# Kernel optimization log

Hardware: AMD Instinct MI355X
Metric: run time of the kernel (lower is better)

## Reference

```python
import jax, jax.numpy as jnp
import numpy as np

B, L, D, H, E = 32, 100, 128, 8, 64
C = D // H
NEG_SLOPE = 0.2
MASK_VAL = -1e9
LN_EPS = 1e-5


def _glorot(key, shape):
    fan_in, fan_out = shape[-1], shape[-2]
    std = np.sqrt(6.0 / (fan_in + fan_out))
    return jax.random.uniform(key, shape, jnp.float32, -std, std)


def setup_inputs() -> dict:
    key = jax.random.key(0)
    ks = jax.random.split(key, 12)
    x = jax.random.normal(ks[0], (B, L, D), jnp.float32)
    adj = jax.random.randint(ks[1], (B, L, L), 0, 2, jnp.int32)
    e = jax.random.normal(ks[2], (B, L, L, E), jnp.float32)
    Wx = _glorot(ks[3], (D, D))          # linear_x weight (out, in)
    We = _glorot(ks[4], (D, E))          # linear_e weight (out, in)
    att_src = _glorot(ks[5], (H, C))
    att_dst = _glorot(ks[6], (H, C))
    att_e = _glorot(ks[7], (H, C))
    ffn_w = _glorot(ks[8], (D, D))
    ffn_b = jnp.zeros((D,), jnp.float32)
    ln_g = jnp.ones((D,), jnp.float32)
    ln_b = jnp.zeros((D,), jnp.float32)
    return dict(x=x, adj=adj, e=e, Wx=Wx, We=We, att_src=att_src,
                att_dst=att_dst, att_e=att_e, ffn_w=ffn_w, ffn_b=ffn_b,
                ln_g=ln_g, ln_b=ln_b)


def reference(x, adj, e, Wx, We, att_src, att_dst, att_e, ffn_w, ffn_b, ln_g, ln_b):
    Bb, Ll, Dd = x.shape
    Hh, Cc = att_src.shape
    # node / edge projections
    xp = (x @ Wx.T).reshape(Bb, Ll, Hh, Cc)                      # (B,L,H,C)
    ep = jnp.einsum('bije,de->bijd', e, We).reshape(Bb, Ll, Ll, Hh, Cc)  # (B,L,L,H,C)
    # per-head attention logits
    xj = jnp.einsum('blhc,hc->blh', xp, att_src)                 # source score
    xi = jnp.einsum('blhc,hc->blh', xp, att_dst)                 # dest score
    es = jnp.einsum('bijhc,hc->bijh', ep, att_e)                 # edge score
    s = xi[:, :, None, :] + xj[:, None, :, :] + es               # (B,L,L,H)
    s = jax.nn.leaky_relu(s, NEG_SLOPE)
    s = jnp.where((adj != 0)[..., None], s, MASK_VAL)
    alpha = jax.nn.softmax(s, axis=2)                            # softmax over j
    # aggregation: out[b,i,h,c] = sum_j alpha[b,i,j,h] * xp[b,j,h,c]
    out = jnp.einsum('bijh,bjhc->bihc', alpha, xp).reshape(Bb, Ll, Dd)
    # FFN: linear -> layernorm -> relu (dropout p=0)
    h = out @ ffn_w.T + ffn_b
    mu = h.mean(-1, keepdims=True)
    var = jnp.mean((h - mu) ** 2, axis=-1, keepdims=True)
    h = (h - mu) * jax.lax.rsqrt(var + LN_EPS) * ln_g + ln_b
    return jax.nn.relu(h)
```

## Files before the change

kernel.cpp:

```cpp
#include <hip/hip_runtime.h>
#include <hip/hip_bf16.h>

#define NB 32
#define NL 100
#define ND 128
#define NH 8
#define NE 64
#define NC 16

#define WS_WXT  0
#define WS_WFT  16384
#define WS_PROJ 32768
#define WS_XI   33280
#define WS_XJ   58880
#define WS_XP   84480
#define WS_ES   (84480 + NB * NL * ND)
#define WS_TOT  (WS_ES + NB * NL * NL * NH)

__device__ float g_ws[WS_TOT];

static __device__ __forceinline__ float pick8(const float* a, int c) {
    return (c < 4)
        ? ((c < 2) ? (c == 0 ? a[0] : a[1]) : (c == 2 ? a[2] : a[3]))
        : ((c < 6) ? (c == 4 ? a[4] : a[5]) : (c == 6 ? a[6] : a[7]));
}

__global__ __launch_bounds__(256) void prep_kernel(
        const float* __restrict__ Wx, const float* __restrict__ We,
        const float* __restrict__ att_e, const float* __restrict__ ffn_w) {
    int gid = blockIdx.x * 256 + threadIdx.x;
    if (gid < 16384) {
        int k = gid >> 7, d = gid & 127;
        g_ws[WS_WXT + gid] = Wx[d * 128 + k];
        g_ws[WS_WFT + gid] = ffn_w[d * 128 + k];
    } else if (gid < 16384 + 512) {
        int pid = gid - 16384;
        int h = pid >> 6, eix = pid & 63;
        float acc = 0.f;
        #pragma unroll
        for (int c = 0; c < NC; ++c)
            acc += att_e[h * NC + c] * We[(h * NC + c) * NE + eix];
        g_ws[WS_PROJ + pid] = acc;
    }
}

__global__ __launch_bounds__(256) void mega2_kernel(
        const float* __restrict__ x, const float* __restrict__ e,
        const float* __restrict__ att_src, const float* __restrict__ att_dst) {
    __shared__ float xrowL[8][128];
    int blk = blockIdx.x;
    int t = threadIdx.x;

    if (blk < 400) {
        int hb = t >> 7;
        int tl = t & 127;
        int bl0 = blk * 8 + hb * 4;
        #pragma unroll
        for (int r = 0; r < 4; ++r)
            xrowL[hb * 4 + r][tl] = x[(bl0 + r) * 128 + tl];
        __syncthreads();
        const float* WxT = g_ws + WS_WXT;
        float acc0 = 0.f, acc1 = 0.f, acc2 = 0.f, acc3 = 0.f;
        #pragma unroll 8
        for (int k = 0; k < 128; ++k) {
            float wv = WxT[k * 128 + tl];
            acc0 = fmaf(xrowL[hb * 4 + 0][k], wv, acc0);
            acc1 = fmaf(xrowL[hb * 4 + 1][k], wv, acc1);
            acc2 = fmaf(xrowL[hb * 4 + 2][k], wv, acc2);
            acc3 = fmaf(xrowL[hb * 4 + 3][k], wv, acc3);
        }
        float accs[4] = {acc0, acc1, acc2, acc3};
        float asr = att_src[tl], adt = att_dst[tl];
        #pragma unroll
        for (int r = 0; r < 4; ++r) {
            g_ws[WS_XP + (bl0 + r) * 128 + tl] = accs[r];
            float sp = accs[r] * asr;
            float sd = accs[r] * adt;
            #pragma unroll
            for (int st = 1; st < 16; st <<= 1) {
                sp += __shfl_xor(sp, st);
                sd += __shfl_xor(sd, st);
            }
            if ((tl & 15) == 0) {
                g_ws[WS_XJ + (bl0 + r) * 8 + (tl >> 4)] = sp;
                g_ws[WS_XI + (bl0 + r) * 8 + (tl >> 4)] = sd;
            }
        }
    } else {
        const float4* proj4 = (const float4*)(g_ws + WS_PROJ);
        int lane = t & 63;
        int j_sub = lane >> 3, c_sub = lane & 7;
        float4 p4[16];
        #pragma unroll
        for (int h = 0; h < 8; ++h) {
            p4[h * 2]     = proj4[h * 16 + c_sub * 2];
            p4[h * 2 + 1] = proj4[h * 16 + c_sub * 2 + 1];
        }
        const float4* e4 = (const float4*)e;
        int wid = (blk - 400) * 4 + (t >> 6);
        const int nw = 2048 * 4;
        for (int chunk = wid; chunk < NB * NL * NL / 8; chunk += nw) {
            long rid = (long)chunk * 8 + j_sub;
            float4 ev0 = e4[rid * 16 + c_sub * 2];
            float4 ev1 = e4[rid * 16 + c_sub * 2 + 1];
            float part[8];
            #pragma unroll
            for (int h = 0; h < 8; ++h) {
                float4 a = p4[h * 2], bq = p4[h * 2 + 1];
                part[h] = ev0.x * a.x + ev0.y * a.y + ev0.z * a.z + ev0.w * a.w
                        + ev1.x * bq.x + ev1.y * bq.y + ev1.z * bq.z + ev1.w * bq.w;
            }
            #pragma unroll
            for (int st = 1; st < 8; st <<= 1)
                #pragma unroll
                for (int h = 0; h < 8; ++h)
                    part[h] += __shfl_xor(part[h], st);
            g_ws[WS_ES + rid * 8 + c_sub] = pick8(part, c_sub);
        }
    }
}

__global__ __launch_bounds__(256) void gat_main(
        const int* __restrict__ adj, const float* __restrict__ ffn_b,
        const float* __restrict__ ln_g, const float* __restrict__ ln_b,
        float* __restrict__ out) {
    __shared__ float s_lds[2][NL * 9];
    __shared__ float partL[2][2][128];
    __shared__ float rowL[2][128];
    __shared__ float hvalL[2][128];
    __shared__ float inv[2][8];
    __shared__ float mr[2][2];

    int blk = blockIdx.x;
    int b = blk / 50, i0 = (blk % 50) * 2;
    int t = threadIdx.x;
    const float* xp = g_ws + WS_XP;

    {
        int h = t & 7, jj = t >> 3;
        #pragma unroll
        for (int ii = 0; ii < 2; ++ii) {
            int bi = b * NL + i0 + ii;
            float xiv = g_ws[WS_XI + bi * 8 + h];
            #pragma unroll
            for (int r = 0; r < 4; ++r) {
                int j = jj + r * 32;
                if (j < NL) {
                    float s = xiv + g_ws[WS_XJ + (b * NL + j) * 8 + h]
                            + g_ws[WS_ES + ((long)bi * NL + j) * 8 + h];
                    s = s > 0.f ? s : 0.2f * s;
                    s = adj[bi * NL + j] ? s : -1e9f;
                    s_lds[ii][j * 9 + h] = s;
                }
            }
        }
    }
    __syncthreads();
    {
        int h = t >> 5, jt = t & 31;
        const float LOG2E = 1.44269504f;
        #pragma unroll
        for (int ii = 0; ii < 2; ++ii) {
            float* sl = s_lds[ii];
            float v0 = sl[jt * 9 + h];
            float v1 = sl[(jt + 32) * 9 + h];
            float v2 = sl[(jt + 64) * 9 + h];
            float v3 = (jt < 4) ? sl[(jt + 96) * 9 + h] : -3.0e38f;
            float m = fmaxf(fmaxf(v0, v1), fmaxf(v2, v3));
            #pragma unroll
            for (int st = 1; st < 32; st <<= 1) m = fmaxf(m, __shfl_xor(m, st));
            float p0 = exp2f((v0 - m) * LOG2E);
            float p1 = exp2f((v1 - m) * LOG2E);
            float p2 = exp2f((v2 - m) * LOG2E);
            float p3 = (jt < 4) ? exp2f((v3 - m) * LOG2E) : 0.f;
            float sum = p0 + p1 + p2 + p3;
            #pragma unroll
            for (int st = 1; st < 32; st <<= 1) sum += __shfl_xor(sum, st);
            sl[jt * 9 + h] = p0;
            sl[(jt + 32) * 9 + h] = p1;
            sl[(jt + 64) * 9 + h] = p2;
            if (jt < 4) sl[(jt + 96) * 9 + h] = p3;
            if (jt == 0) inv[ii][h] = 1.0f / sum;
        }
    }
    __syncthreads();
    {
        int d = t & 127, half = t >> 7, hh = d >> 4;
        float a0 = 0.f, a1 = 0.f;
        int j0 = half * 50;
        #pragma unroll 5
        for (int k = 0; k < 50; ++k) {
            int j = j0 + k;
            float xv = xp[(b * NL + j) * 128 + d];
            a0 = fmaf(s_lds[0][j * 9 + hh], xv, a0);
            a1 = fmaf(s_lds[1][j * 9 + hh], xv, a1);
        }
        partL[half][0][d] = a0;
        partL[half][1][d] = a1;
    }
    __syncthreads();
    {
        int d = t & 127, ii = t >> 7;
        rowL[ii][d] = (partL[0][ii][d] + partL[1][ii][d]) * inv[ii][d >> 4];
    }
    __syncthreads();
    {
        int d = t & 127, half = t >> 7;
        const float* WfT = g_ws + WS_WFT;
        float a0 = 0.f, a1 = 0.f;
        int k0 = half * 64;
        #pragma unroll 8
        for (int k = k0; k < k0 + 64; ++k) {
            float wv = WfT[k * 128 + d];
            a0 = fmaf(wv, rowL[0][k], a0);
            a1 = fmaf(wv, rowL[1][k], a1);
        }
        partL[half][0][d] = a0;
        partL[half][1][d] = a1;
    }
    __syncthreads();
    {
        int d = t & 127, ii = t >> 7;
        hvalL[ii][d] = partL[0][ii][d] + partL[1][ii][d] + ffn_b[d];
    }
    __syncthreads();
    {
        int row = t >> 6, lane = t & 63;
        if (row < 2) {
            float a = hvalL[row][lane], b2 = hvalL[row][lane + 64];
            float s1 = a + b2, s2 = a * a + b2 * b2;
            #pragma unroll
            for (int st = 1; st < 64; st <<= 1) {
                s1 += __shfl_xor(s1, st);
                s2 += __shfl_xor(s2, st);
            }
            if (lane == 0) {
                float mu = s1 * (1.0f / 128.0f);
                float var = s2 * (1.0f / 128.0f) - mu * mu;
                mr[row][0] = mu;
                mr[row][1] = rsqrtf(var + 1e-5f);
            }
        }
    }
    __syncthreads();
    {
        int d = t & 127, ii = t >> 7;
        float y = (hvalL[ii][d] - mr[ii][0]) * mr[ii][1] * ln_g[d] + ln_b[d];
        out[(b * NL + i0 + ii) * 128 + d] = fmaxf(y, 0.f);
    }
}

extern "C" void kernel_launch(void* const* d_in, const int* in_sizes, int n_in,
                              void* d_out, int out_size, void* d_ws, size_t ws_size,
                              hipStream_t stream) {
    const float* x       = (const float*)d_in[0];
    const int*   adj     = (const int*)  d_in[1];
    const float* e       = (const float*)d_in[2];
    const float* Wx      = (const float*)d_in[3];
    const float* We      = (const float*)d_in[4];
    const float* att_src = (const float*)d_in[5];
    const float* att_dst = (const float*)d_in[6];
    const float* att_e   = (const float*)d_in[7];
    const float* ffn_w   = (const float*)d_in[8];
    const float* ffn_b   = (const float*)d_in[9];
    const float* ln_g    = (const float*)d_in[10];
    const float* ln_b    = (const float*)d_in[11];
    float* out = (float*)d_out;

    hipLaunchKernelGGL(prep_kernel, dim3(66), dim3(256), 0, stream,
                       Wx, We, att_e, ffn_w);
    hipLaunchKernelGGL(mega2_kernel, dim3(2448), dim3(256), 0, stream,
                       x, e, att_src, att_dst);
    hipLaunchKernelGGL(gat_main, dim3(NB * 50), dim3(256), 0, stream,
                       adj, ffn_b, ln_g, ln_b, out);
}
```

Baseline: 180.3 us.

## Fold weight prep kernel into projection kernel, removing a launch

```diff
diff --git a/kernel.cpp b/kernel.cpp
--- a/kernel.cpp
+++ b/kernel.cpp
@@ -8,9 +8,7 @@
 #define NE 64
 #define NC 16
 
-#define WS_WXT  0
 #define WS_WFT  16384
-#define WS_PROJ 32768
 #define WS_XI   33280
 #define WS_XJ   58880
 #define WS_XP   84480
@@ -25,80 +23,112 @@
         : ((c < 6) ? (c == 4 ? a[4] : a[5]) : (c == 6 ? a[6] : a[7]));
 }
 
-__global__ __launch_bounds__(256) void prep_kernel(
+__global__ __launch_bounds__(256) void mega3_kernel(
+        const float* __restrict__ x, const float* __restrict__ e,
         const float* __restrict__ Wx, const float* __restrict__ We,
+        const float* __restrict__ att_src, const float* __restrict__ att_dst,
         const float* __restrict__ att_e, const float* __restrict__ ffn_w) {
-    int gid = blockIdx.x * 256 + threadIdx.x;
-    if (gid < 16384) {
-        int k = gid >> 7, d = gid & 127;
-        g_ws[WS_WXT + gid] = Wx[d * 128 + k];
-        g_ws[WS_WFT + gid] = ffn_w[d * 128 + k];
-    } else if (gid < 16384 + 512) {
-        int pid = gid - 16384;
-        int h = pid >> 6, eix = pid & 63;
-        float acc = 0.f;
-        #pragma unroll
-        for (int c = 0; c < NC; ++c)
-            acc += att_e[h * NC + c] * We[(h * NC + c) * NE + eix];
-        g_ws[WS_PROJ + pid] = acc;
-    }
-}
-
-__global__ __launch_bounds__(256) void mega2_kernel(
-        const float* __restrict__ x, const float* __restrict__ e,
-        const float* __restrict__ att_src, const float* __restrict__ att_dst) {
-    __shared__ float xrowL[8][128];
+    __shared__ float smem[2048];
     int blk = blockIdx.x;
     int t = threadIdx.x;
 
     if (blk < 400) {
-        int hb = t >> 7;
-        int tl = t & 127;
-        int bl0 = blk * 8 + hb * 4;
-        #pragma unroll
-        for (int r = 0; r < 4; ++r)
-            xrowL[hb * 4 + r][tl] = x[(bl0 + r) * 128 + tl];
+        int bl0 = blk * 8;
+        float* xrowL = smem;
+        float* xpL   = smem + 1024;
+        ((float4*)xrowL)[t] = ((const float4*)(x + bl0 * 128))[t];
         __syncthreads();
-        const float* WxT = g_ws + WS_WXT;
-        float acc0 = 0.f, acc1 = 0.f, acc2 = 0.f, acc3 = 0.f;
-        #pragma unroll 8
-        for (int k = 0; k < 128; ++k) {
-            float wv = WxT[k * 128 + tl];
-            acc0 = fmaf(xrowL[hb * 4 + 0][k], wv, acc0);
-            acc1 = fmaf(xrowL[hb * 4 + 1][k], wv, acc1);
-            acc2 = fmaf(xrowL[hb * 4 + 2][k], wv, acc2);
-            acc3 = fmaf(xrowL[hb * 4 + 3][k], wv, acc3);
-        }
-        float accs[4] = {acc0, acc1, acc2, acc3};
-        float asr = att_src[tl], adt = att_dst[tl];
-        #pragma unroll
-        for (int r = 0; r < 4; ++r) {
-            g_ws[WS_XP + (bl0 + r) * 128 + tl] = accs[r];
-            float sp = accs[r] * asr;
-            float sd = accs[r] * adt;
-            #pragma unroll
-            for (int st = 1; st < 16; st <<= 1) {
-                sp += __shfl_xor(sp, st);
-                sd += __shfl_xor(sd, st);
-            }
-            if ((tl & 15) == 0) {
-                g_ws[WS_XJ + (bl0 + r) * 8 + (tl >> 4)] = sp;
-                g_ws[WS_XI + (bl0 + r) * 8 + (tl >> 4)] = sd;
-            }
+        int lane = t & 63, w = t >> 6;
+        int d_sub = lane >> 3, c_sub = lane & 7;
+        const float4* Wx4 = (const float4*)Wx;
+        #pragma unroll
+        for (int rr = 0; rr < 4; ++rr) {
+            int d = rr * 32 + w * 8 + d_sub;
+            float4 wc0 = Wx4[d * 32 + c_sub * 4 + 0];
+            float4 wc1 = Wx4[d * 32 + c_sub * 4 + 1];
+            float4 wc2 = Wx4[d * 32 + c_sub * 4 + 2];
+            float4 wc3 = Wx4[d * 32 + c_sub * 4 + 3];
+            float accs[8];
+            #pragma unroll
+            for (int r = 0; r < 8; ++r) {
+                const float4* xr = (const float4*)(xrowL + r * 128);
+                float4 a0 = xr[c_sub * 4 + 0], a1 = xr[c_sub * 4 + 1];
+                float4 a2 = xr[c_sub * 4 + 2], a3 = xr[c_sub * 4 + 3];
+                accs[r] = wc0.x * a0.x + wc0.y * a0.y + wc0.z * a0.z + wc0.w * a0.w
+                        + wc1.x * a1.x + wc1.y * a1.y + wc1.z * a1.z + wc1.w * a1.w
+                        + wc2.x * a2.x + wc2.y * a2.y + wc2.z * a2.z + wc2.w * a2.w
+                        + wc3.x * a3.x + wc3.y * a3.y + wc3.z * a3.z + wc3.w * a3.w;
+            }
+            #pragma unroll
+            for (int st = 1; st < 8; st <<= 1)
+                #pragma unroll
+                for (int r = 0; r < 8; ++r)
+                    accs[r] += __shfl_xor(accs[r], st);
+            float v = pick8(accs, c_sub);
+            xpL[c_sub * 128 + d] = v;
+            g_ws[WS_XP + (bl0 + c_sub) * 128 + d] = v;
+        }
+        __syncthreads();
+        {
+            int r = t >> 5, sub = t & 31;
+            int h = sub >> 2;
+            float sp = 0.f, sd = 0.f;
+            #pragma unroll
+            for (int q = 0; q < 4; ++q) {
+                float xv = xpL[r * 128 + sub * 4 + q];
+                sp += xv * att_src[sub * 4 + q];
+                sd += xv * att_dst[sub * 4 + q];
+            }
+            sp += __shfl_xor(sp, 1); sp += __shfl_xor(sp, 2);
+            sd += __shfl_xor(sd, 1); sd += __shfl_xor(sd, 2);
+            if ((sub & 3) == 0) {
+                g_ws[WS_XJ + (bl0 + r) * 8 + h] = sp;
+                g_ws[WS_XI + (bl0 + r) * 8 + h] = sd;
+            }
+        }
+    } else if (blk < 416) {
+        int r0 = (blk - 400) * 8;
+        float* tileL = smem;
+        int k = t & 127, rh = t >> 7;
+        #pragma unroll
+        for (int ri = 0; ri < 4; ++ri) {
+            int rr = ri * 2 + rh;
+            tileL[rr * 128 + k] = ffn_w[(r0 + rr) * 128 + k];
+        }
+        __syncthreads();
+        if (t < 128) {
+            float4 p0, p1;
+            p0.x = tileL[0 * 128 + t]; p0.y = tileL[1 * 128 + t];
+            p0.z = tileL[2 * 128 + t]; p0.w = tileL[3 * 128 + t];
+            p1.x = tileL[4 * 128 + t]; p1.y = tileL[5 * 128 + t];
+            p1.z = tileL[6 * 128 + t]; p1.w = tileL[7 * 128 + t];
+            float4* dst = (float4*)(g_ws + WS_WFT + t * 128 + r0);
+            dst[0] = p0;
+            dst[1] = p1;
         }
     } else {
-        const float4* proj4 = (const float4*)(g_ws + WS_PROJ);
+        float* projL = smem;
+        for (int pid = t; pid < 512; pid += 256) {
+            int h = pid >> 6, eix = pid & 63;
+            float acc = 0.f;
+            #pragma unroll
+            for (int c = 0; c < NC; ++c)
+                acc += att_e[h * NC + c] * We[(h * NC + c) * NE + eix];
+            projL[pid] = acc;
+        }
+        __syncthreads();
         int lane = t & 63;
         int j_sub = lane >> 3, c_sub = lane & 7;
+        const float4* projL4 = (const float4*)projL;
         float4 p4[16];
         #pragma unroll
         for (int h = 0; h < 8; ++h) {
-            p4[h * 2]     = proj4[h * 16 + c_sub * 2];
-            p4[h * 2 + 1] = proj4[h * 16 + c_sub * 2 + 1];
+            p4[h * 2]     = projL4[h * 16 + c_sub * 2];
+            p4[h * 2 + 1] = projL4[h * 16 + c_sub * 2 + 1];
         }
         const float4* e4 = (const float4*)e;
-        int wid = (blk - 400) * 4 + (t >> 6);
-        const int nw = 2048 * 4;
+        int wid = (blk - 416) * 4 + (t >> 6);
+        const int nw = 1632 * 4;
         for (int chunk = wid; chunk < NB * NL * NL / 8; chunk += nw) {
             long rid = (long)chunk * 8 + j_sub;
             float4 ev0 = e4[rid * 16 + c_sub * 2];
@@ -267,10 +297,8 @@
     const float* ln_b    = (const float*)d_in[11];
     float* out = (float*)d_out;
 
-    hipLaunchKernelGGL(prep_kernel, dim3(66), dim3(256), 0, stream,
-                       Wx, We, att_e, ffn_w);
-    hipLaunchKernelGGL(mega2_kernel, dim3(2448), dim3(256), 0, stream,
-                       x, e, att_src, att_dst);
+    hipLaunchKernelGGL(mega3_kernel, dim3(2048), dim3(256), 0, stream,
+                       x, e, Wx, We, att_src, att_dst, att_e, ffn_w);
     hipLaunchKernelGGL(gat_main, dim3(NB * 50), dim3(256), 0, stream,
                        adj, ffn_b, ln_g, ln_b, out);
 }
```

Result: no change. 181.5 us (+0.7%).
